# Performance work log

Hardware: AMD Instinct MI355X
Metric: run time of the kernel (lower is better)

## Reference

```python
import jax, jax.numpy as jnp
import numpy as np

N, DIM, K = 65536, 256, 4096

def setup_inputs() -> dict:
    key = jax.random.key(0)
    kx, kc = jax.random.split(key)
    x = jax.random.normal(kx, (N, DIM), dtype=jnp.float32)
    codebook = jax.random.normal(kc, (K, DIM), dtype=jnp.float32) * 0.02
    return {"x": x, "codebook": codebook}

def reference(x, codebook):
    # torch.cdist(x, codebook).argmin(-1) == argmin of squared distances;
    x_sq = jnp.sum(x * x, axis=-1, keepdims=True)           # (n, 1)
    c_sq = jnp.sum(codebook * codebook, axis=-1)            # (k,)
    dots = jnp.einsum('nd,kd->nk', x, codebook)             # (n, k) GEMM
    dist_sq = x_sq - 2.0 * dots + c_sq[None, :]             # (n, k)
    indices = jnp.argmin(dist_sq, axis=-1)                  # (n,)
    quantized = jnp.take(codebook, indices, axis=0)         # (n, dim) gather
    return (quantized, indices)
```

## Files before the change

kernel.cpp:

```cpp
#include <hip/hip_runtime.h>
#include <cfloat>

typedef _Float16 half8 __attribute__((ext_vector_type(8)));
typedef float    f32x4 __attribute__((ext_vector_type(4)));

#define N_ROWS 65536
#define DIM    256
#define KCODES 4096
#define BM 128
#define BN 128
#define BK 32

#define WS_CSQ 0
#define WS_XSQ 16384
#define WS_CH  278528
#define WS_CL  2375680

__global__ void prep_codes(const float* __restrict__ cb, float* __restrict__ csq,
                           _Float16* __restrict__ ch, _Float16* __restrict__ cl) {
    int c = blockIdx.x * blockDim.x + threadIdx.x;
    if (c >= KCODES) return;
    const float* row = cb + (size_t)c * DIM;
    float s = 0.f;
    for (int k = 0; k < DIM; k += 4) {
        float4 v = *(const float4*)&row[k];
        s = fmaf(v.x, v.x, s); s = fmaf(v.y, v.y, s);
        s = fmaf(v.z, v.z, s); s = fmaf(v.w, v.w, s);
        float sv[4] = {v.x * 64.f, v.y * 64.f, v.z * 64.f, v.w * 64.f};
        #pragma unroll
        for (int j = 0; j < 4; ++j) {
            _Float16 h = (_Float16)sv[j];
            ch[(size_t)c * DIM + k + j] = h;
            cl[(size_t)c * DIM + k + j] = (_Float16)(sv[j] - (float)h);
        }
    }
    csq[c] = s;
}

__global__ void prep_xsq(const float* __restrict__ x, float* __restrict__ xsq) {
    __shared__ float  As[32 * DIM];
    __shared__ double dtmp[128];
    const int t = threadIdx.x;
    const int n0 = blockIdx.x * 32;
    #pragma unroll
    for (int i = 0; i < 8; ++i) {
        int r = 4 * i + (t >> 6), d4 = (t & 63) * 4;
        *(float4*)&As[r * DIM + d4] = *(const float4*)&x[(size_t)(n0 + r) * DIM + d4];
    }
    __syncthreads();
    if (t < 128) {
        int r = t >> 2, part = t & 3;
        const float* ap = &As[r * DIM + 64 * part];
        double s = 0.0;
        for (int k = 0; k < 64; ++k) { double v = (double)ap[k]; s = fma(v, v, s); }
        dtmp[t] = s;
    }
    __syncthreads();
    if (t < 32)
        xsq[n0 + t] = (float)((dtmp[4*t] + dtmp[4*t+1]) + (dtmp[4*t+2] + dtmp[4*t+3]));
}

__global__ __launch_bounds__(256, 2)
void vq_mfma(const float* __restrict__ x, const float* __restrict__ cb,
             const float* __restrict__ csq, const float* __restrict__ xsq,
             const _Float16* __restrict__ ch, const _Float16* __restrict__ cl,
             float* __restrict__ out_q, float* __restrict__ out_idx) {
    __shared__ _Float16 AhS[BM * BK], AlS[BM * BK], BhS[BN * BK], BlS[BN * BK];

    const int t = threadIdx.x;
    const int lane = t & 63, wave = t >> 6;
    const int wy = wave >> 1, wx = wave & 1;
    const int m = lane & 15, q = lane >> 4;
    const int n0 = blockIdx.x * BM;
    const int sr = t >> 1, sh = t & 1;
    const int swz = (q ^ (m & 3)) * 8;

    float xsq_r[16];
    #pragma unroll
    for (int s = 0; s < 16; ++s)
        xsq_r[s] = xsq[n0 + 64 * wy + 16 * (s >> 2) + 4 * q + (s & 3)];

    float best[16]; int bidx[16];
    #pragma unroll
    for (int s = 0; s < 16; ++s) { best[s] = FLT_MAX; bidx[s] = 0; }

    for (int chunk = 0; chunk < KCODES / BN; ++chunk) {
        const int c0 = chunk * BN;
        float csq_c[4];
        #pragma unroll
        for (int tc = 0; tc < 4; ++tc) csq_c[tc] = csq[c0 + 64 * wx + 16 * tc + m];

        f32x4 acc[4][4];
        #pragma unroll
        for (int tr = 0; tr < 4; ++tr)
            #pragma unroll
            for (int tc = 0; tc < 4; ++tc) acc[tr][tc] = (f32x4){0.f, 0.f, 0.f, 0.f};

        for (int sl = 0; sl < DIM / BK; ++sl) {
            const int ks = sl * BK;
            __syncthreads();
            {
                const float* asrc = &x[(size_t)(n0 + sr) * DIM + ks + 16 * sh];
                float av[16];
                *(float4*)&av[0]  = *(const float4*)(asrc + 0);
                *(float4*)&av[4]  = *(const float4*)(asrc + 4);
                *(float4*)&av[8]  = *(const float4*)(asrc + 8);
                *(float4*)&av[12] = *(const float4*)(asrc + 12);
                half8 h0, h1, l0, l1;
                #pragma unroll
                for (int j = 0; j < 8; ++j) {
                    _Float16 h = (_Float16)av[j];
                    h0[j] = h; l0[j] = (_Float16)(av[j] - (float)h);
                    _Float16 g = (_Float16)av[j + 8];
                    h1[j] = g; l1[j] = (_Float16)(av[j + 8] - (float)g);
                }
                const int base = sr * BK, sw = sr & 3;
                const int g0 = 2 * sh, g1 = 2 * sh + 1;
                *(half8*)&AhS[base + ((g0 ^ sw) * 8)] = h0;
                *(half8*)&AhS[base + ((g1 ^ sw) * 8)] = h1;
                *(half8*)&AlS[base + ((g0 ^ sw) * 8)] = l0;
                *(half8*)&AlS[base + ((g1 ^ sw) * 8)] = l1;
            }
            {
                const _Float16* bhs = &ch[(size_t)(c0 + sr) * DIM + ks + 16 * sh];
                const _Float16* bls = &cl[(size_t)(c0 + sr) * DIM + ks + 16 * sh];
                half8 h0 = *(const half8*)(bhs), h1 = *(const half8*)(bhs + 8);
                half8 l0 = *(const half8*)(bls), l1 = *(const half8*)(bls + 8);
                const int base = sr * BK, sw = sr & 3;
                const int g0 = 2 * sh, g1 = 2 * sh + 1;
                *(half8*)&BhS[base + ((g0 ^ sw) * 8)] = h0;
                *(half8*)&BhS[base + ((g1 ^ sw) * 8)] = h1;
                *(half8*)&BlS[base + ((g0 ^ sw) * 8)] = l0;
                *(half8*)&BlS[base + ((g1 ^ sw) * 8)] = l1;
            }
            __syncthreads();

            half8 aH[4], aL[4], bH[4], bL[4];
            #pragma unroll
            for (int tr = 0; tr < 4; ++tr) {
                int off = (64 * wy + 16 * tr + m) * BK + swz;
                aH[tr] = *(const half8*)&AhS[off];
                aL[tr] = *(const half8*)&AlS[off];
            }
            #pragma unroll
            for (int tc = 0; tc < 4; ++tc) {
                int off = (64 * wx + 16 * tc + m) * BK + swz;
                bH[tc] = *(const half8*)&BhS[off];
                bL[tc] = *(const half8*)&BlS[off];
            }
            #pragma unroll
            for (int tc = 0; tc < 4; ++tc)
                #pragma unroll
                for (int tr = 0; tr < 4; ++tr)
                    acc[tr][tc] = __builtin_amdgcn_mfma_f32_16x16x32_f16(aH[tr], bH[tc], acc[tr][tc], 0, 0, 0);
            #pragma unroll
            for (int tc = 0; tc < 4; ++tc)
                #pragma unroll
                for (int tr = 0; tr < 4; ++tr)
                    acc[tr][tc] = __builtin_amdgcn_mfma_f32_16x16x32_f16(aH[tr], bL[tc], acc[tr][tc], 0, 0, 0);
            #pragma unroll
            for (int tc = 0; tc < 4; ++tc)
                #pragma unroll
                for (int tr = 0; tr < 4; ++tr)
                    acc[tr][tc] = __builtin_amdgcn_mfma_f32_16x16x32_f16(aL[tr], bH[tc], acc[tr][tc], 0, 0, 0);
        }
        #pragma unroll
        for (int tc = 0; tc < 4; ++tc) {
            int c = c0 + 64 * wx + 16 * tc + m;
            #pragma unroll
            for (int tr = 0; tr < 4; ++tr) {
                #pragma unroll
                for (int e = 0; e < 4; ++e) {
                    float dot = acc[tr][tc][e] * 0.015625f;
                    float d = fmaf(-2.f, dot, xsq_r[tr * 4 + e]) + csq_c[tc];
                    int s = tr * 4 + e;
                    if (d < best[s]) { best[s] = d; bidx[s] = c; }
                }
            }
        }
    }

    #pragma unroll
    for (int s = 0; s < 16; ++s) {
        float v = best[s]; int idx = bidx[s];
        #pragma unroll
        for (int off = 1; off < 16; off <<= 1) {
            float v2 = __shfl_xor(v, off);
            int   i2 = __shfl_xor(idx, off);
            if (v2 < v || (v2 == v && i2 < idx)) { v = v2; idx = i2; }
        }
        best[s] = v; bidx[s] = idx;
    }
    __syncthreads();
    float* rb = (float*)BhS;
    int*   ri = (int*)BlS;
    {
        int s = m;
        int row_local = 64 * wy + 16 * (s >> 2) + 4 * q + (s & 3);
        rb[row_local * 2 + wx] = best[s];
        ri[row_local * 2 + wx] = bidx[s];
    }
    __syncthreads();
    int* widx = (int*)AhS;
    if (t < BM) {
        float d0 = rb[t * 2], d1 = rb[t * 2 + 1];
        int   i0 = ri[t * 2], i1 = ri[t * 2 + 1];
        int w = (d1 < d0 || (d1 == d0 && i1 < i0)) ? i1 : i0;
        widx[t] = w;
        out_idx[n0 + t] = (float)w;
    }
    __syncthreads();
    const int l4 = t & 63, rg = t >> 6;
    #pragma unroll 4
    for (int i = 0; i < 32; ++i) {
        int r = rg + 4 * i;
        *(float4*)&out_q[(size_t)(n0 + r) * DIM + l4 * 4] =
            *(const float4*)&cb[(size_t)widx[r] * DIM + l4 * 4];
    }
}

extern "C" void kernel_launch(void* const* d_in, const int* in_sizes, int n_in,
                              void* d_out, int out_size, void* d_ws, size_t ws_size,
                              hipStream_t stream) {
    const float* x  = (const float*)d_in[0];
    const float* cb = (const float*)d_in[1];
    float* out_q   = (float*)d_out;
    float* out_idx = (float*)d_out + (size_t)N_ROWS * DIM;

    float*    csq = (float*)((char*)d_ws + WS_CSQ);
    float*    xsq = (float*)((char*)d_ws + WS_XSQ);
    _Float16* ch  = (_Float16*)((char*)d_ws + WS_CH);
    _Float16* cl  = (_Float16*)((char*)d_ws + WS_CL);

    prep_codes<<<KCODES / 256, 256, 0, stream>>>(cb, csq, ch, cl);
    prep_xsq<<<N_ROWS / 32, 256, 0, stream>>>(x, xsq);
    vq_mfma<<<N_ROWS / BM, 256, 0, stream>>>(x, cb, csq, xsq, ch, cl, out_q, out_idx);
}
```

Baseline: 623.8 us.

## Pre-split x to fp16 hi/lo in output buffer and double-buffer tiles via global_load_lds

The prep kernel now converts x into fp16 hi/lo halves and writes them into the output buffer as scratch space, so the main kernel no longer converts fp32 to split fp16 every k-slice. The main kernel loads A and B tiles straight from global memory into double-buffered LDS with global_load_lds and prefetches the next slice while running the MFMAs on the current one, leaving one barrier per slice instead of two. The epilogue overwrites the scratch rows with gathered codes, and each block reads only its own rows, so the reuse is safe. The cost is twice the LDS footprint and extra global traffic for the pre-split x.

```diff
diff --git a/kernel.cpp b/kernel.cpp
--- a/kernel.cpp
+++ b/kernel.cpp
@@ -10,11 +10,17 @@
 #define BM 128
 #define BN 128
 #define BK 32
+#define NSLICE (DIM / BK)
+#define NCHUNK (KCODES / BN)
 
 #define WS_CSQ 0
 #define WS_XSQ 16384
 #define WS_CH  278528
 #define WS_CL  2375680
+
+#define GLDS(g, l) __builtin_amdgcn_global_load_lds(                       \
+    (const __attribute__((address_space(1))) unsigned int*)(g),            \
+    (__attribute__((address_space(3))) unsigned int*)(l), 16, 0, 0)
 
 __global__ void prep_codes(const float* __restrict__ cb, float* __restrict__ csq,
                            _Float16* __restrict__ ch, _Float16* __restrict__ cl) {
@@ -37,7 +43,8 @@
     csq[c] = s;
 }
 
-__global__ void prep_xsq(const float* __restrict__ x, float* __restrict__ xsq) {
+__global__ void prep_xsq(const float* __restrict__ x, float* __restrict__ xsq,
+                         char* __restrict__ xq) {
     __shared__ float  As[32 * DIM];
     __shared__ double dtmp[128];
     const int t = threadIdx.x;
@@ -48,6 +55,25 @@
         *(float4*)&As[r * DIM + d4] = *(const float4*)&x[(size_t)(n0 + r) * DIM + d4];
     }
     __syncthreads();
+    {
+        const int r = t >> 3;
+        const int col8 = (t & 7) * 8;
+        char* dst = xq + (((size_t)(n0 + r)) << 10) + (size_t)(col8 * 2);
+        const float* src = &As[r * DIM + col8];
+        #pragma unroll
+        for (int i = 0; i < 4; ++i) {
+            half8 hv, lv;
+            #pragma unroll
+            for (int j = 0; j < 8; ++j) {
+                float v = src[i * 64 + j];
+                _Float16 h = (_Float16)v;
+                hv[j] = h;
+                lv[j] = (_Float16)(v - (float)h);
+            }
+            *(half8*)(dst + i * 128) = hv;
+            *(half8*)(dst + 512 + i * 128) = lv;
+        }
+    }
     if (t < 128) {
         int r = t >> 2, part = t & 3;
         const float* ap = &As[r * DIM + 64 * part];
@@ -61,19 +87,52 @@
 }
 
 __global__ __launch_bounds__(256, 2)
-void vq_mfma(const float* __restrict__ x, const float* __restrict__ cb,
+void vq_mfma(const float* __restrict__ cb,
              const float* __restrict__ csq, const float* __restrict__ xsq,
              const _Float16* __restrict__ ch, const _Float16* __restrict__ cl,
-             float* __restrict__ out_q, float* __restrict__ out_idx) {
-    __shared__ _Float16 AhS[BM * BK], AlS[BM * BK], BhS[BN * BK], BlS[BN * BK];
+             float* out_q, float* __restrict__ out_idx) {
+    __shared__ _Float16 AhS[2 * BM * BK], AlS[2 * BM * BK];
+    __shared__ _Float16 BhS[2 * BN * BK], BlS[2 * BN * BK];
 
     const int t = threadIdx.x;
     const int lane = t & 63, wave = t >> 6;
     const int wy = wave >> 1, wx = wave & 1;
     const int m = lane & 15, q = lane >> 4;
     const int n0 = blockIdx.x * BM;
-    const int sr = t >> 1, sh = t & 1;
     const int swz = (q ^ (m & 3)) * 8;
+
+    const int rq  = lane >> 2;
+    const int gph = lane & 3;
+    const int glogB = ((gph ^ (rq & 3)) << 4);
+    const char* xqb = (const char*)out_q;
+    const char* aBase  = xqb + (((size_t)(n0 + wave * 32 + rq)) << 10) + glogB;
+    const char* bBaseH = (const char*)ch + (((size_t)(wave * 32 + rq)) << 9) + glogB;
+    const char* bBaseL = (const char*)cl + (((size_t)(wave * 32 + rq)) << 9) + glogB;
+
+#define STAGE(ck2, sl2, nb) do {                                             \
+    const char* a_  = aBase  + (size_t)((sl2) * 64);                         \
+    const size_t bo_ = ((size_t)(ck2) << 16) + (size_t)((sl2) * 64);         \
+    const char* bh_ = bBaseH + bo_;                                          \
+    const char* bl_ = bBaseL + bo_;                                          \
+    _Float16* Ah_ = AhS + (nb) * (BM * BK) + wave * (32 * BK);               \
+    _Float16* Al_ = AlS + (nb) * (BM * BK) + wave * (32 * BK);               \
+    _Float16* Bh_ = BhS + (nb) * (BN * BK) + wave * (32 * BK);               \
+    _Float16* Bl_ = BlS + (nb) * (BN * BK) + wave * (32 * BK);               \
+    GLDS(a_,           Ah_);                                                 \
+    GLDS(a_ + 16384,   Ah_ + 16 * BK);                                       \
+    GLDS(a_ + 512,     Al_);                                                 \
+    GLDS(a_ + 16896,   Al_ + 16 * BK);                                       \
+    GLDS(bh_,          Bh_);                                                 \
+    GLDS(bh_ + 8192,   Bh_ + 16 * BK);                                       \
+    GLDS(bl_,          Bl_);                                                 \
+    GLDS(bl_ + 8192,   Bl_ + 16 * BK);                                       \
+} while (0)
+
+    int aoffs[4], boffs[4];
+    #pragma unroll
+    for (int tr = 0; tr < 4; ++tr) aoffs[tr] = (64 * wy + 16 * tr + m) * BK + swz;
+    #pragma unroll
+    for (int tc = 0; tc < 4; ++tc) boffs[tc] = (64 * wx + 16 * tc + m) * BK + swz;
 
     float xsq_r[16];
     #pragma unroll
@@ -84,7 +143,11 @@
     #pragma unroll
     for (int s = 0; s < 16; ++s) { best[s] = FLT_MAX; bidx[s] = 0; }
 
-    for (int chunk = 0; chunk < KCODES / BN; ++chunk) {
+    STAGE(0, 0, 0);
+    asm volatile("s_waitcnt vmcnt(0)" ::: "memory");
+    __syncthreads();
+
+    for (int chunk = 0; chunk < NCHUNK; ++chunk) {
         const int c0 = chunk * BN;
         float csq_c[4];
         #pragma unroll
@@ -96,57 +159,29 @@
             #pragma unroll
             for (int tc = 0; tc < 4; ++tc) acc[tr][tc] = (f32x4){0.f, 0.f, 0.f, 0.f};
 
-        for (int sl = 0; sl < DIM / BK; ++sl) {
-            const int ks = sl * BK;
-            __syncthreads();
-            {
-                const float* asrc = &x[(size_t)(n0 + sr) * DIM + ks + 16 * sh];
-                float av[16];
-                *(float4*)&av[0]  = *(const float4*)(asrc + 0);
-                *(float4*)&av[4]  = *(const float4*)(asrc + 4);
-                *(float4*)&av[8]  = *(const float4*)(asrc + 8);
-                *(float4*)&av[12] = *(const float4*)(asrc + 12);
-                half8 h0, h1, l0, l1;
-                #pragma unroll
-                for (int j = 0; j < 8; ++j) {
-                    _Float16 h = (_Float16)av[j];
-                    h0[j] = h; l0[j] = (_Float16)(av[j] - (float)h);
-                    _Float16 g = (_Float16)av[j + 8];
-                    h1[j] = g; l1[j] = (_Float16)(av[j + 8] - (float)g);
-                }
-                const int base = sr * BK, sw = sr & 3;
-                const int g0 = 2 * sh, g1 = 2 * sh + 1;
-                *(half8*)&AhS[base + ((g0 ^ sw) * 8)] = h0;
-                *(half8*)&AhS[base + ((g1 ^ sw) * 8)] = h1;
-                *(half8*)&AlS[base + ((g0 ^ sw) * 8)] = l0;
-                *(half8*)&AlS[base + ((g1 ^ sw) * 8)] = l1;
-            }
-            {
-                const _Float16* bhs = &ch[(size_t)(c0 + sr) * DIM + ks + 16 * sh];
-                const _Float16* bls = &cl[(size_t)(c0 + sr) * DIM + ks + 16 * sh];
-                half8 h0 = *(const half8*)(bhs), h1 = *(const half8*)(bhs + 8);
-                half8 l0 = *(const half8*)(bls), l1 = *(const half8*)(bls + 8);
-                const int base = sr * BK, sw = sr & 3;
-                const int g0 = 2 * sh, g1 = 2 * sh + 1;
-                *(half8*)&BhS[base + ((g0 ^ sw) * 8)] = h0;
-                *(half8*)&BhS[base + ((g1 ^ sw) * 8)] = h1;
-                *(half8*)&BlS[base + ((g0 ^ sw) * 8)] = l0;
-                *(half8*)&BlS[base + ((g1 ^ sw) * 8)] = l1;
-            }
-            __syncthreads();
+        #pragma unroll
+        for (int sl = 0; sl < NSLICE; ++sl) {
+            if (sl < NSLICE - 1) {
+                STAGE(chunk, sl + 1, (sl + 1) & 1);
+            } else if (chunk < NCHUNK - 1) {
+                STAGE(chunk + 1, 0, 0);
+            }
+            const int cbuf = sl & 1;
+            const _Float16* Ahr = AhS + cbuf * (BM * BK);
+            const _Float16* Alr = AlS + cbuf * (BM * BK);
+            const _Float16* Bhr = BhS + cbuf * (BN * BK);
+            const _Float16* Blr = BlS + cbuf * (BN * BK);
 
             half8 aH[4], aL[4], bH[4], bL[4];
             #pragma unroll
             for (int tr = 0; tr < 4; ++tr) {
-                int off = (64 * wy + 16 * tr + m) * BK + swz;
-                aH[tr] = *(const half8*)&AhS[off];
-                aL[tr] = *(const half8*)&AlS[off];
+                aH[tr] = *(const half8*)&Ahr[aoffs[tr]];
+                aL[tr] = *(const half8*)&Alr[aoffs[tr]];
             }
             #pragma unroll
             for (int tc = 0; tc < 4; ++tc) {
-                int off = (64 * wx + 16 * tc + m) * BK + swz;
-                bH[tc] = *(const half8*)&BhS[off];
-                bL[tc] = *(const half8*)&BlS[off];
+                bH[tc] = *(const half8*)&Bhr[boffs[tc]];
+                bL[tc] = *(const half8*)&Blr[boffs[tc]];
             }
             #pragma unroll
             for (int tc = 0; tc < 4; ++tc)
@@ -163,20 +198,25 @@
                 #pragma unroll
                 for (int tr = 0; tr < 4; ++tr)
                     acc[tr][tc] = __builtin_amdgcn_mfma_f32_16x16x32_f16(aL[tr], bH[tc], acc[tr][tc], 0, 0, 0);
-        }
-        #pragma unroll
-        for (int tc = 0; tc < 4; ++tc) {
-            int c = c0 + 64 * wx + 16 * tc + m;
-            #pragma unroll
-            for (int tr = 0; tr < 4; ++tr) {
-                #pragma unroll
-                for (int e = 0; e < 4; ++e) {
-                    float dot = acc[tr][tc][e] * 0.015625f;
-                    float d = fmaf(-2.f, dot, xsq_r[tr * 4 + e]) + csq_c[tc];
-                    int s = tr * 4 + e;
-                    if (d < best[s]) { best[s] = d; bidx[s] = c; }
+
+            if (sl == NSLICE - 1) {
+                #pragma unroll
+                for (int tc = 0; tc < 4; ++tc) {
+                    int c = c0 + 64 * wx + 16 * tc + m;
+                    #pragma unroll
+                    for (int tr = 0; tr < 4; ++tr) {
+                        #pragma unroll
+                        for (int e = 0; e < 4; ++e) {
+                            float dot = acc[tr][tc][e] * 0.015625f;
+                            float d = fmaf(-2.f, dot, xsq_r[tr * 4 + e]) + csq_c[tc];
+                            int s = tr * 4 + e;
+                            if (d < best[s]) { best[s] = d; bidx[s] = c; }
+                        }
+                    }
                 }
             }
+            asm volatile("s_waitcnt vmcnt(0)" ::: "memory");
+            __syncthreads();
         }
     }
 
@@ -217,6 +257,7 @@
         *(float4*)&out_q[(size_t)(n0 + r) * DIM + l4 * 4] =
             *(const float4*)&cb[(size_t)widx[r] * DIM + l4 * 4];
     }
+#undef STAGE
 }
 
 extern "C" void kernel_launch(void* const* d_in, const int* in_sizes, int n_in,
@@ -233,6 +274,6 @@
     _Float16* cl  = (_Float16*)((char*)d_ws + WS_CL);
 
     prep_codes<<<KCODES / 256, 256, 0, stream>>>(cb, csq, ch, cl);
-    prep_xsq<<<N_ROWS / 32, 256, 0, stream>>>(x, xsq);
-    vq_mfma<<<N_ROWS / BM, 256, 0, stream>>>(x, cb, csq, xsq, ch, cl, out_q, out_idx);
-}
+    prep_xsq<<<N_ROWS / 32, 256, 0, stream>>>(x, xsq, (char*)out_q);
+    vq_mfma<<<N_ROWS / BM, 256, 0, stream>>>(cb, csq, xsq, ch, cl, out_q, out_idx);
+}
```

Result: slower. 645.7 us (+3.5%).
